# Performance work log

Measured on AMD Instinct MI355X. Metric: run time of the kernel, lower is better.

## Reference

```python
import jax, jax.numpy as jnp
import numpy as np

D_MODEL = 1024
N_HEADS = 16
D_FF = 4096
HEAD_DIM = D_MODEL // N_HEADS
LN_EPS = 1e-5


def layer_norm(x, g, b):
    m = jnp.mean(x, axis=-1, keepdims=True)
    v = jnp.mean(jnp.square(x - m), axis=-1, keepdims=True)
    return (x - m) * jax.lax.rsqrt(v + LN_EPS) * g + b


def setup_inputs() -> dict:
    key = jax.random.key(0)
    ks = jax.random.split(key, 16)
    s = 0.02
    d = {
        'x': jax.random.normal(ks[0], (4, 2048, D_MODEL), jnp.float32),
        'Wq': jax.random.normal(ks[1], (D_MODEL, D_MODEL), jnp.float32) * s,
        'bq': jnp.zeros((D_MODEL,), jnp.float32),
        'Wk': jax.random.normal(ks[2], (D_MODEL, D_MODEL), jnp.float32) * s,
        'bk': jnp.zeros((D_MODEL,), jnp.float32),
        'Wv': jax.random.normal(ks[3], (D_MODEL, D_MODEL), jnp.float32) * s,
        'bv': jnp.zeros((D_MODEL,), jnp.float32),
        'Wo': jax.random.normal(ks[4], (D_MODEL, D_MODEL), jnp.float32) * s,
        'bo': jnp.zeros((D_MODEL,), jnp.float32),
        'W1': jax.random.normal(ks[5], (D_FF, D_MODEL), jnp.float32) * s,
        'b1': jnp.zeros((D_FF,), jnp.float32),
        'W2': jax.random.normal(ks[6], (D_MODEL, D_FF), jnp.float32) * s,
        'b2': jnp.zeros((D_MODEL,), jnp.float32),
        'g1': jnp.ones((D_MODEL,), jnp.float32),
        'be1': jnp.zeros((D_MODEL,), jnp.float32),
        'g2': jnp.ones((D_MODEL,), jnp.float32),
        'be2': jnp.zeros((D_MODEL,), jnp.float32),
    }
    return d


def reference(x, Wq, bq, Wk, bk, Wv, bv, Wo, bo, W1, b1, W2, b2, g1, be1, g2, be2):
    B, S, D = x.shape
    H, hd = N_HEADS, HEAD_DIM
    # QKV projections; chunk along d_model -> heads (same as reshape last dim)
    q = (x @ Wq.T + bq).reshape(B, S, H, hd)
    k = (x @ Wk.T + bk).reshape(B, S, H, hd)
    v = (x @ Wv.T + bv).reshape(B, S, H, hd)
    # scaled dot-product attention (no mask, dropout = identity in eval)
    scores = jnp.einsum('bqhd,bkhd->bhqk', q, k) / jnp.sqrt(jnp.float32(hd))
    attn = jax.nn.softmax(scores, axis=-1)
    ctx = jnp.einsum('bhqk,bkhd->bqhd', attn, v).reshape(B, S, D)
    out1 = ctx @ Wo.T + bo
    out = layer_norm(x + out1, g1, be1)
    out2 = jax.nn.relu(out @ W1.T + b1) @ W2.T + b2
    # NOTE: faithful to source bug: second residual uses out1, not out
    return layer_norm(out1 + out2, g2, be2)
```

## Files before the change

### kernel.cpp

```cpp
#include <hip/hip_runtime.h>

typedef __bf16 bf16_t;
typedef __bf16 bf16x8 __attribute__((ext_vector_type(8)));
typedef __bf16 bf16x4 __attribute__((ext_vector_type(4)));
typedef float  f32x4  __attribute__((ext_vector_type(4)));

#define SEQ   2048
#define DMODEL 1024
#define DFF   4096
#define NHEAD 16
#define HDIM  64
#define MTOK  8192

#define MB (size_t)(1024*1024)
static const size_t XB_OFF   = 0;
static const size_t Q_OFF    = 16*MB;
static const size_t K_OFF    = 32*MB;
static const size_t VT_OFF   = 48*MB;
static const size_t FFN1_OFF = 0;
static const size_t CTX_OFF  = 64*MB;
static const size_t OUT1_OFF = 80*MB;
static const size_t LN1_OFF  = 112*MB;
static const size_t WQ_OFF   = 128*MB;
static const size_t WK_OFF   = 130*MB;
static const size_t WV_OFF   = 132*MB;
static const size_t WO_OFF   = 134*MB;
static const size_t W1_OFF   = 136*MB;
static const size_t W2_OFF   = 144*MB;

__device__ inline void gload16(const void* g, void* l) {
    __builtin_amdgcn_global_load_lds((__attribute__((address_space(1))) void*)g,
                                     (__attribute__((address_space(3))) void*)l, 16, 0, 0);
}

__global__ __launch_bounds__(256) void cast_bf16_k(const float* __restrict__ s,
                                                   bf16_t* __restrict__ d, int n8) {
    int i = blockIdx.x * 256 + threadIdx.x;
    if (i >= n8) return;
    float4 v0 = ((const float4*)s)[2*i];
    float4 v1 = ((const float4*)s)[2*i+1];
    bf16x8 o;
    o[0]=(bf16_t)v0.x; o[1]=(bf16_t)v0.y; o[2]=(bf16_t)v0.z; o[3]=(bf16_t)v0.w;
    o[4]=(bf16_t)v1.x; o[5]=(bf16_t)v1.y; o[6]=(bf16_t)v1.z; o[7]=(bf16_t)v1.w;
    *(bf16x8*)(d + (size_t)i*8) = o;
}

template<int EPI>
__global__ __launch_bounds__(256, 2) void gemm_bt(
    const bf16_t* __restrict__ A, const bf16_t* __restrict__ Bm,
    const float* __restrict__ bias, void* __restrict__ out,
    const float* __restrict__ aux, int M, int N, int K, float scale)
{
    __shared__ bf16_t As[128*64];
    __shared__ bf16_t Bs[128*64];
    const int tid = threadIdx.x;
    const int l   = tid & 63;
    const int wid = tid >> 6;
    const int wm  = wid >> 1, wn = wid & 1;
    const int c16 = l & 15,   g  = l >> 4;
    const long brow = (long)blockIdx.y * 128;
    const long bcol = (long)blockIdx.x * 128;

    f32x4 acc[4][4] = {};

    const int nkt = K >> 6;
    for (int kt = 0; kt < nkt; ++kt) {
        __syncthreads();
        const bf16_t* Ag = A  + brow * K + kt*64;
        const bf16_t* Bg = Bm + bcol * K + kt*64;
#pragma unroll
        for (int c = 0; c < 4; ++c) {
            int e   = (c*256 + tid) * 8;
            int row = e >> 6;
            int col = e & 63;
            gload16(Ag + (long)row*K + col, &As[e]);
            gload16(Bg + (long)row*K + col, &Bs[e]);
        }
        __syncthreads();
#pragma unroll
        for (int kk = 0; kk < 2; ++kk) {
            bf16x8 af[4], bfr[4];
#pragma unroll
            for (int mi = 0; mi < 4; ++mi)
                af[mi] = *(const bf16x8*)&As[(wm*64 + mi*16 + c16)*64 + kk*32 + 8*g];
#pragma unroll
            for (int ni = 0; ni < 4; ++ni)
                bfr[ni] = *(const bf16x8*)&Bs[(wn*64 + ni*16 + c16)*64 + kk*32 + 8*g];
#pragma unroll
            for (int mi = 0; mi < 4; ++mi)
#pragma unroll
                for (int ni = 0; ni < 4; ++ni)
                    acc[mi][ni] = __builtin_amdgcn_mfma_f32_16x16x32_bf16(
                        af[mi], bfr[ni], acc[mi][ni], 0, 0, 0);
        }
    }

#pragma unroll
    for (int ni = 0; ni < 4; ++ni) {
        const long c = bcol + wn*64 + ni*16 + c16;
        const float bv = bias[c];
#pragma unroll
        for (int mi = 0; mi < 4; ++mi) {
#pragma unroll
            for (int i = 0; i < 4; ++i) {
                const long r = brow + wm*64 + mi*16 + g*4 + i;
                float v = (acc[mi][ni][i] + bv) * scale;
                if constexpr (EPI == 0) {
                    long off = (((r >> 11)*NHEAD + (c >> 6))*SEQ + (r & (SEQ-1)))*HDIM + (c & 63);
                    ((bf16_t*)out)[off] = (bf16_t)v;
                } else if constexpr (EPI == 1) {
                    long off = (((r >> 11)*NHEAD + (c >> 6))*HDIM + (c & 63))*SEQ + (r & (SEQ-1));
                    ((bf16_t*)out)[off] = (bf16_t)v;
                } else if constexpr (EPI == 2) {
                    ((float*)out)[r*N + c] = v;
                } else if constexpr (EPI == 3) {
                    ((bf16_t*)out)[r*N + c] = (bf16_t)fmaxf(v, 0.f);
                } else {
                    ((float*)out)[r*N + c] = v + aux[r*N + c];
                }
            }
        }
    }
}

__device__ __forceinline__ void kload(bf16x8 (&dst)[4][2], const bf16_t* kb0,
                                      int ktt, int c16, int g) {
    const bf16_t* kbase = kb0 + (size_t)ktt*64*HDIM;
#pragma unroll
    for (int jk = 0; jk < 4; ++jk)
#pragma unroll
        for (int ks = 0; ks < 2; ++ks)
            dst[jk][ks] = *(const bf16x8*)(kbase + (size_t)(16*jk + c16)*HDIM + ks*32 + 8*g);
}

__device__ __forceinline__ void vload(bf16x8 (&vr)[4][2], const bf16_t* vt0,
                                      int ktt, int c16, int g) {
#pragma unroll
    for (int nf = 0; nf < 4; ++nf)
#pragma unroll
        for (int ks = 0; ks < 2; ++ks)
            vr[nf][ks] = *(const bf16x8*)(vt0 + (size_t)(16*nf + c16)*SEQ + ktt*64 + ks*32 + 8*g);
}

__device__ __forceinline__ void attn_step(
    const bf16x8 (&kr)[4][2], const bf16x8 (&vr)[4][2], const bf16x8 (&aq)[2][2],
    f32x4 (&acc)[2][4], float (&m)[2], float (&ls)[2],
    char* myP, int c16, int g)
{
    f32x4 s[2][4];
    const f32x4 z = {0.f, 0.f, 0.f, 0.f};
    __builtin_amdgcn_s_setprio(1);
#pragma unroll
    for (int qf = 0; qf < 2; ++qf)
#pragma unroll
        for (int jk = 0; jk < 4; ++jk) {
            s[qf][jk] = __builtin_amdgcn_mfma_f32_16x16x32_bf16(kr[jk][0], aq[qf][0], z, 0, 0, 0);
            s[qf][jk] = __builtin_amdgcn_mfma_f32_16x16x32_bf16(kr[jk][1], aq[qf][1], s[qf][jk], 0, 0, 0);
        }
    __builtin_amdgcn_s_setprio(0);
#pragma unroll
    for (int qf = 0; qf < 2; ++qf) {
        float a0 = fmaxf(fmaxf(s[qf][0][0], s[qf][0][1]), fmaxf(s[qf][0][2], s[qf][0][3]));
        float a1 = fmaxf(fmaxf(s[qf][1][0], s[qf][1][1]), fmaxf(s[qf][1][2], s[qf][1][3]));
        float a2 = fmaxf(fmaxf(s[qf][2][0], s[qf][2][1]), fmaxf(s[qf][2][2], s[qf][2][3]));
        float a3 = fmaxf(fmaxf(s[qf][3][0], s[qf][3][1]), fmaxf(s[qf][3][2], s[qf][3][3]));
        float pm = fmaxf(fmaxf(a0, a1), fmaxf(a2, a3));
        pm = fmaxf(pm, __shfl_xor(pm, 16, 64));
        pm = fmaxf(pm, __shfl_xor(pm, 32, 64));
        if (__any(pm > m[qf] + 8.0f)) {
            float mn   = fmaxf(m[qf], pm);
            float corr = __expf(m[qf] - mn);
            ls[qf] *= corr;
            m[qf]   = mn;
            float c0 = __shfl(corr, 4*g + 0, 64);
            float c1 = __shfl(corr, 4*g + 1, 64);
            float c2 = __shfl(corr, 4*g + 2, 64);
            float c3 = __shfl(corr, 4*g + 3, 64);
#pragma unroll
            for (int nf = 0; nf < 4; ++nf) {
                acc[qf][nf][0] *= c0; acc[qf][nf][1] *= c1;
                acc[qf][nf][2] *= c2; acc[qf][nf][3] *= c3;
            }
        }
        float rsum = 0.f;
#pragma unroll
        for (int jk = 0; jk < 4; ++jk)
#pragma unroll
            for (int i = 0; i < 4; ++i) {
                s[qf][jk][i] = __expf(s[qf][jk][i] - m[qf]);
                rsum += s[qf][jk][i];
            }
        rsum += __shfl_xor(rsum, 16, 64);
        rsum += __shfl_xor(rsum, 32, 64);
        ls[qf] += rsum;
    }
#pragma unroll
    for (int qf = 0; qf < 2; ++qf)
#pragma unroll
        for (int jk = 0; jk < 4; ++jk) {
            bf16x4 pk;
            pk[0]=(bf16_t)s[qf][jk][0]; pk[1]=(bf16_t)s[qf][jk][1];
            pk[2]=(bf16_t)s[qf][jk][2]; pk[3]=(bf16_t)s[qf][jk][3];
            *(bf16x4*)(myP + (qf*16 + c16)*128 + ((32*jk + 8*g) ^ ((c16 & 7) << 4))) = pk;
        }
    asm volatile("s_waitcnt lgkmcnt(0)" ::: "memory");
    __builtin_amdgcn_sched_barrier(0);
    __builtin_amdgcn_s_setprio(1);
#pragma unroll
    for (int qf = 0; qf < 2; ++qf)
#pragma unroll
        for (int ks = 0; ks < 2; ++ks) {
            bf16x8 pa = *(const bf16x8*)(myP + (qf*16 + c16)*128 + ((ks*64 + 16*g) ^ ((c16 & 7) << 4)));
#pragma unroll
            for (int nf = 0; nf < 4; ++nf)
                acc[qf][nf] = __builtin_amdgcn_mfma_f32_16x16x32_bf16(pa, vr[nf][ks], acc[qf][nf], 0, 0, 0);
        }
    __builtin_amdgcn_s_setprio(0);
    asm volatile("" ::: "memory");
}

__global__ __launch_bounds__(256, 2) void attn_k(
    const bf16_t* __restrict__ qb, const bf16_t* __restrict__ kb,
    const bf16_t* __restrict__ vt, bf16_t* __restrict__ ctx)
{
    const int bh = blockIdx.y;
    const int w  = threadIdx.x >> 6;
    const int l  = threadIdx.x & 63;
    const int c16 = l & 15, g = l >> 4;
    const int q0 = blockIdx.x*128 + w*32;

    __shared__ char Ps[4*8192];
    char* myP = &Ps[w*8192];

    bf16x8 aq[2][2];
#pragma unroll
    for (int qf = 0; qf < 2; ++qf) {
        const bf16_t* qrow = qb + ((size_t)bh*SEQ + q0 + qf*16 + c16)*HDIM;
        aq[qf][0] = *(const bf16x8*)(qrow + 8*g);
        aq[qf][1] = *(const bf16x8*)(qrow + 32 + 8*g);
    }

    const bf16_t* kb0 = kb + (size_t)bh*SEQ*HDIM;
    const bf16_t* vt0 = vt + (size_t)bh*HDIM*SEQ;

    f32x4 acc[2][4] = {};
    float m[2]  = {-1e30f, -1e30f};
    float ls[2] = {0.f, 0.f};

    bf16x8 kA[4][2], kB[4][2], vr[4][2];
    kload(kA, kb0, 0, c16, g);
    for (int kt = 0; kt < SEQ/64; kt += 2) {
        kload(kB, kb0, kt + 1, c16, g);
        vload(vr, vt0, kt, c16, g);
        attn_step(kA, vr, aq, acc, m, ls, myP + (kt & 1)*4096, c16, g);
        kload(kA, kb0, (kt + 2 < SEQ/64) ? kt + 2 : 0, c16, g);
        vload(vr, vt0, kt + 1, c16, g);
        attn_step(kB, vr, aq, acc, m, ls, myP + ((kt + 1) & 1)*4096, c16, g);
    }

    const int b = bh >> 4, h = bh & 15;
#pragma unroll
    for (int qf = 0; qf < 2; ++qf) {
        float i0 = 1.0f / __shfl(ls[qf], 4*g + 0, 64);
        float i1 = 1.0f / __shfl(ls[qf], 4*g + 1, 64);
        float i2 = 1.0f / __shfl(ls[qf], 4*g + 2, 64);
        float i3 = 1.0f / __shfl(ls[qf], 4*g + 3, 64);
#pragma unroll
        for (int nf = 0; nf < 4; ++nf) {
            long col = (size_t)h*HDIM + nf*16 + c16;
            long rb  = (size_t)b*SEQ + q0 + qf*16 + 4*g;
            ctx[(rb + 0)*DMODEL + col] = (bf16_t)(acc[qf][nf][0] * i0);
            ctx[(rb + 1)*DMODEL + col] = (bf16_t)(acc[qf][nf][1] * i1);
            ctx[(rb + 2)*DMODEL + col] = (bf16_t)(acc[qf][nf][2] * i2);
            ctx[(rb + 3)*DMODEL + col] = (bf16_t)(acc[qf][nf][3] * i3);
        }
    }
}

__global__ __launch_bounds__(256) void ln_k(
    const float* __restrict__ a, const float* __restrict__ b,
    const float* __restrict__ g, const float* __restrict__ be,
    float* __restrict__ of, bf16_t* __restrict__ ob)
{
    const long row = blockIdx.x;
    const int tid = threadIdx.x;
    float4 v = ((const float4*)(a + row*DMODEL))[tid];
    if (b) {
        float4 u = ((const float4*)(b + row*DMODEL))[tid];
        v.x += u.x; v.y += u.y; v.z += u.z; v.w += u.w;
    }
    float s = v.x + v.y + v.z + v.w;
    float q = v.x*v.x + v.y*v.y + v.z*v.z + v.w*v.w;
#pragma unroll
    for (int msk = 1; msk < 64; msk <<= 1) {
        s += __shfl_xor(s, msk, 64);
        q += __shfl_xor(q, msk, 64);
    }
    __shared__ float sb[4], qb2[4];
    int w = tid >> 6, lid = tid & 63;
    if (lid == 0) { sb[w] = s; qb2[w] = q; }
    __syncthreads();
    s = sb[0] + sb[1] + sb[2] + sb[3];
    q = qb2[0] + qb2[1] + qb2[2] + qb2[3];
    float mean = s * (1.f/1024.f);
    float var  = q * (1.f/1024.f) - mean*mean;
    float rs   = rsqrtf(var + 1e-5f);
    float4 gv = ((const float4*)g)[tid];
    float4 bv = ((const float4*)be)[tid];
    float o0 = (v.x-mean)*rs*gv.x + bv.x;
    float o1 = (v.y-mean)*rs*gv.y + bv.y;
    float o2 = (v.z-mean)*rs*gv.z + bv.z;
    float o3 = (v.w-mean)*rs*gv.w + bv.w;
    if (ob) {
        bf16x4 o; o[0]=(bf16_t)o0; o[1]=(bf16_t)o1; o[2]=(bf16_t)o2; o[3]=(bf16_t)o3;
        *(bf16x4*)(ob + row*DMODEL + tid*4) = o;
    } else {
        float4 o = make_float4(o0, o1, o2, o3);
        ((float4*)(of + row*DMODEL))[tid] = o;
    }
}

extern "C" void kernel_launch(void* const* d_in, const int* in_sizes, int n_in,
                              void* d_out, int out_size, void* d_ws, size_t ws_size,
                              hipStream_t stream)
{
    const float* x   = (const float*)d_in[0];
    const float* Wq  = (const float*)d_in[1];
    const float* bq  = (const float*)d_in[2];
    const float* Wk  = (const float*)d_in[3];
    const float* bk  = (const float*)d_in[4];
    const float* Wv  = (const float*)d_in[5];
    const float* bvv = (const float*)d_in[6];
    const float* Wo  = (const float*)d_in[7];
    const float* bo  = (const float*)d_in[8];
    const float* W1  = (const float*)d_in[9];
    const float* b1  = (const float*)d_in[10];
    const float* W2  = (const float*)d_in[11];
    const float* b2  = (const float*)d_in[12];
    const float* g1  = (const float*)d_in[13];
    const float* be1 = (const float*)d_in[14];
    const float* g2  = (const float*)d_in[15];
    const float* be2 = (const float*)d_in[16];

    char* ws = (char*)d_ws;
    bf16_t* xb   = (bf16_t*)(ws + XB_OFF);
    bf16_t* qbuf = (bf16_t*)(ws + Q_OFF);
    bf16_t* kbuf = (bf16_t*)(ws + K_OFF);
    bf16_t* vtb  = (bf16_t*)(ws + VT_OFF);
    bf16_t* ffn1 = (bf16_t*)(ws + FFN1_OFF);
    bf16_t* ctxb = (bf16_t*)(ws + CTX_OFF);
    float*  out1 = (float*)(ws + OUT1_OFF);
    bf16_t* ln1b = (bf16_t*)(ws + LN1_OFF);
    bf16_t* wqb  = (bf16_t*)(ws + WQ_OFF);
    bf16_t* wkb  = (bf16_t*)(ws + WK_OFF);
    bf16_t* wvb  = (bf16_t*)(ws + WV_OFF);
    bf16_t* wob  = (bf16_t*)(ws + WO_OFF);
    bf16_t* w1b  = (bf16_t*)(ws + W1_OFF);
    bf16_t* w2b  = (bf16_t*)(ws + W2_OFF);
    float*  dout = (float*)d_out;

    auto cast = [&](const float* s, bf16_t* d, long n) {
        int n8 = (int)(n / 8);
        cast_bf16_k<<<(n8 + 255)/256, 256, 0, stream>>>(s, d, n8);
    };
    cast(x,  xb,  (long)MTOK*DMODEL);
    cast(Wq, wqb, (long)DMODEL*DMODEL);
    cast(Wk, wkb, (long)DMODEL*DMODEL);
    cast(Wv, wvb, (long)DMODEL*DMODEL);
    cast(Wo, wob, (long)DMODEL*DMODEL);
    cast(W1, w1b, (long)DFF*DMODEL);
    cast(W2, w2b, (long)DMODEL*DFF);

    dim3 blk(256);
    gemm_bt<0><<<dim3(DMODEL/128, MTOK/128), blk, 0, stream>>>(xb, wqb, bq, qbuf, nullptr, MTOK, DMODEL, DMODEL, 0.125f);
    gemm_bt<0><<<dim3(DMODEL/128, MTOK/128), blk, 0, stream>>>(xb, wkb, bk, kbuf, nullptr, MTOK, DMODEL, DMODEL, 1.f);
    gemm_bt<1><<<dim3(DMODEL/128, MTOK/128), blk, 0, stream>>>(xb, wvb, bvv, vtb, nullptr, MTOK, DMODEL, DMODEL, 1.f);
    attn_k<<<dim3(SEQ/128, 4*NHEAD), blk, 0, stream>>>(qbuf, kbuf, vtb, ctxb);
    gemm_bt<2><<<dim3(DMODEL/128, MTOK/128), blk, 0, stream>>>(ctxb, wob, bo, out1, nullptr, MTOK, DMODEL, DMODEL, 1.f);
    ln_k<<<MTOK, blk, 0, stream>>>(x, out1, g1, be1, nullptr, ln1b);
    gemm_bt<3><<<dim3(DFF/128, MTOK/128), blk, 0, stream>>>(ln1b, w1b, b1, ffn1, nullptr, MTOK, DFF, DMODEL, 1.f);
    gemm_bt<4><<<dim3(DMODEL/128, MTOK/128), blk, 0, stream>>>(ffn1, w2b, b2, out1, out1, MTOK, DMODEL, DFF, 1.f);
    ln_k<<<MTOK, blk, 0, stream>>>(out1, nullptr, g2, be2, dout, nullptr);
}
```

Before: 585.8 us.

## Fuse QKV GEMMs, swizzle GEMM tiles, and software-pipeline attention loop

Concatenates Wq/Wk/Wv into one bf16 weight and runs a single QKV GEMM whose epilogue scatters to Q (scaled), K and transposed V, removing two launches and two re-reads of x. Every GEMM now remaps block ids so that consecutive blocks land on different XCDs. The attention kernel uses a 1D grid with a head-interleaved mapping and is restructured into a pipeline that overlaps the QK MFMAs of the next tile with the softmax and PV of the current one, double-buffering K registers. This raises register pressure in attention, and the concatenated bias is staged in the out1 buffer, which is overwritten later.

```diff
diff --git a/kernel.cpp b/kernel.cpp
--- a/kernel.cpp
+++ b/kernel.cpp
@@ -21,9 +21,7 @@
 static const size_t CTX_OFF  = 64*MB;
 static const size_t OUT1_OFF = 80*MB;
 static const size_t LN1_OFF  = 112*MB;
-static const size_t WQ_OFF   = 128*MB;
-static const size_t WK_OFF   = 130*MB;
-static const size_t WV_OFF   = 132*MB;
+static const size_t WQKV_OFF = 128*MB;
 static const size_t WO_OFF   = 134*MB;
 static const size_t W1_OFF   = 136*MB;
 static const size_t W2_OFF   = 144*MB;
@@ -45,10 +43,19 @@
     *(bf16x8*)(d + (size_t)i*8) = o;
 }
 
+__global__ __launch_bounds__(256) void concat_bias_k(const float* __restrict__ a,
+                                                     const float* __restrict__ b,
+                                                     const float* __restrict__ c,
+                                                     float* __restrict__ o) {
+    int i = blockIdx.x * 256 + threadIdx.x;
+    o[i] = (i < 1024) ? a[i] : ((i < 2048) ? b[i - 1024] : c[i - 2048]);
+}
+
 template<int EPI>
 __global__ __launch_bounds__(256, 2) void gemm_bt(
     const bf16_t* __restrict__ A, const bf16_t* __restrict__ Bm,
     const float* __restrict__ bias, void* __restrict__ out,
+    void* __restrict__ out_k, void* __restrict__ out_v,
     const float* __restrict__ aux, int M, int N, int K, float scale)
 {
     __shared__ bf16_t As[128*64];
@@ -58,8 +65,11 @@
     const int wid = tid >> 6;
     const int wm  = wid >> 1, wn = wid & 1;
     const int c16 = l & 15,   g  = l >> 4;
-    const long brow = (long)blockIdx.y * 128;
-    const long bcol = (long)blockIdx.x * 128;
+    int lin = blockIdx.y * gridDim.x + blockIdx.x;
+    int nwg = gridDim.x * gridDim.y;
+    int swz = (lin & 7) * (nwg >> 3) + (lin >> 3);
+    const long brow = (long)(swz / gridDim.x) * 128;
+    const long bcol = (long)(swz % gridDim.x) * 128;
 
     f32x4 acc[4][4] = {};
 
@@ -105,18 +115,23 @@
             for (int i = 0; i < 4; ++i) {
                 const long r = brow + wm*64 + mi*16 + g*4 + i;
                 float v = (acc[mi][ni][i] + bv) * scale;
-                if constexpr (EPI == 0) {
-                    long off = (((r >> 11)*NHEAD + (c >> 6))*SEQ + (r & (SEQ-1)))*HDIM + (c & 63);
-                    ((bf16_t*)out)[off] = (bf16_t)v;
-                } else if constexpr (EPI == 1) {
-                    long off = (((r >> 11)*NHEAD + (c >> 6))*HDIM + (c & 63))*SEQ + (r & (SEQ-1));
-                    ((bf16_t*)out)[off] = (bf16_t)v;
-                } else if constexpr (EPI == 2) {
+                if constexpr (EPI == 2) {
                     ((float*)out)[r*N + c] = v;
                 } else if constexpr (EPI == 3) {
                     ((bf16_t*)out)[r*N + c] = (bf16_t)fmaxf(v, 0.f);
-                } else {
+                } else if constexpr (EPI == 4) {
                     ((float*)out)[r*N + c] = v + aux[r*N + c];
+                } else if constexpr (EPI == 5) {
+                    const int mat = (int)(c >> 10);
+                    const int hc  = (int)(c & 1023);
+                    const long bb = r >> 11, sidx = r & (SEQ-1);
+                    const long hb = bb*NHEAD + (hc >> 6);
+                    if (mat == 0)
+                        ((bf16_t*)out)[(hb*SEQ + sidx)*HDIM + (hc & 63)] = (bf16_t)(v * 0.125f);
+                    else if (mat == 1)
+                        ((bf16_t*)out_k)[(hb*SEQ + sidx)*HDIM + (hc & 63)] = (bf16_t)v;
+                    else
+                        ((bf16_t*)out_v)[(hb*HDIM + (hc & 63))*SEQ + sidx] = (bf16_t)v;
                 }
             }
         }
@@ -142,12 +157,8 @@
             vr[nf][ks] = *(const bf16x8*)(vt0 + (size_t)(16*nf + c16)*SEQ + ktt*64 + ks*32 + 8*g);
 }
 
-__device__ __forceinline__ void attn_step(
-    const bf16x8 (&kr)[4][2], const bf16x8 (&vr)[4][2], const bf16x8 (&aq)[2][2],
-    f32x4 (&acc)[2][4], float (&m)[2], float (&ls)[2],
-    char* myP, int c16, int g)
-{
-    f32x4 s[2][4];
+__device__ __forceinline__ void qk_step(f32x4 (&s)[2][4], const bf16x8 (&kr)[4][2],
+                                        const bf16x8 (&aq)[2][2]) {
     const f32x4 z = {0.f, 0.f, 0.f, 0.f};
     __builtin_amdgcn_s_setprio(1);
 #pragma unroll
@@ -158,6 +169,10 @@
             s[qf][jk] = __builtin_amdgcn_mfma_f32_16x16x32_bf16(kr[jk][1], aq[qf][1], s[qf][jk], 0, 0, 0);
         }
     __builtin_amdgcn_s_setprio(0);
+}
+
+__device__ __forceinline__ void sm_step(f32x4 (&s)[2][4], f32x4 (&acc)[2][4],
+                                        float (&m)[2], float (&ls)[2], int g) {
 #pragma unroll
     for (int qf = 0; qf < 2; ++qf) {
         float a0 = fmaxf(fmaxf(s[qf][0][0], s[qf][0][1]), fmaxf(s[qf][0][2], s[qf][0][3]));
@@ -194,6 +209,9 @@
         rsum += __shfl_xor(rsum, 32, 64);
         ls[qf] += rsum;
     }
+}
+
+__device__ __forceinline__ void pwrite_step(const f32x4 (&s)[2][4], char* buf, int c16, int g) {
 #pragma unroll
     for (int qf = 0; qf < 2; ++qf)
 #pragma unroll
@@ -201,33 +219,37 @@
             bf16x4 pk;
             pk[0]=(bf16_t)s[qf][jk][0]; pk[1]=(bf16_t)s[qf][jk][1];
             pk[2]=(bf16_t)s[qf][jk][2]; pk[3]=(bf16_t)s[qf][jk][3];
-            *(bf16x4*)(myP + (qf*16 + c16)*128 + ((32*jk + 8*g) ^ ((c16 & 7) << 4))) = pk;
-        }
-    asm volatile("s_waitcnt lgkmcnt(0)" ::: "memory");
-    __builtin_amdgcn_sched_barrier(0);
+            *(bf16x4*)(buf + (qf*16 + c16)*128 + ((32*jk + 8*g) ^ ((c16 & 7) << 4))) = pk;
+        }
+}
+
+__device__ __forceinline__ void pv_step(f32x4 (&acc)[2][4], const bf16x8 (&vr)[4][2],
+                                        const char* buf, int c16, int g) {
     __builtin_amdgcn_s_setprio(1);
 #pragma unroll
     for (int qf = 0; qf < 2; ++qf)
 #pragma unroll
         for (int ks = 0; ks < 2; ++ks) {
-            bf16x8 pa = *(const bf16x8*)(myP + (qf*16 + c16)*128 + ((ks*64 + 16*g) ^ ((c16 & 7) << 4)));
+            bf16x8 pa = *(const bf16x8*)(buf + (qf*16 + c16)*128 + ((ks*64 + 16*g) ^ ((c16 & 7) << 4)));
 #pragma unroll
             for (int nf = 0; nf < 4; ++nf)
                 acc[qf][nf] = __builtin_amdgcn_mfma_f32_16x16x32_bf16(pa, vr[nf][ks], acc[qf][nf], 0, 0, 0);
         }
     __builtin_amdgcn_s_setprio(0);
-    asm volatile("" ::: "memory");
 }
 
 __global__ __launch_bounds__(256, 2) void attn_k(
     const bf16_t* __restrict__ qb, const bf16_t* __restrict__ kb,
     const bf16_t* __restrict__ vt, bf16_t* __restrict__ ctx)
 {
-    const int bh = blockIdx.y;
-    const int w  = threadIdx.x >> 6;
-    const int l  = threadIdx.x & 63;
+    const int id  = blockIdx.x;
+    const int idx = id >> 3;
+    const int bh  = (id & 7) + 8 * (idx & 7);
+    const int qt  = idx >> 3;
+    const int w   = threadIdx.x >> 6;
+    const int l   = threadIdx.x & 63;
     const int c16 = l & 15, g = l >> 4;
-    const int q0 = blockIdx.x*128 + w*32;
+    const int q0  = qt*128 + w*32;
 
     __shared__ char Ps[4*8192];
     char* myP = &Ps[w*8192];
@@ -247,16 +269,31 @@
     float m[2]  = {-1e30f, -1e30f};
     float ls[2] = {0.f, 0.f};
 
-    bf16x8 kA[4][2], kB[4][2], vr[4][2];
-    kload(kA, kb0, 0, c16, g);
-    for (int kt = 0; kt < SEQ/64; kt += 2) {
-        kload(kB, kb0, kt + 1, c16, g);
-        vload(vr, vt0, kt, c16, g);
-        attn_step(kA, vr, aq, acc, m, ls, myP + (kt & 1)*4096, c16, g);
-        kload(kA, kb0, (kt + 2 < SEQ/64) ? kt + 2 : 0, c16, g);
-        vload(vr, vt0, kt + 1, c16, g);
-        attn_step(kB, vr, aq, acc, m, ls, myP + ((kt + 1) & 1)*4096, c16, g);
-    }
+    bf16x8 kr[2][4][2], vr[4][2];
+    f32x4 s[2][4];
+
+    kload(kr[0], kb0, 0, c16, g);
+    vload(vr, vt0, 0, c16, g);
+    kload(kr[1], kb0, 1, c16, g);
+    qk_step(s, kr[0], aq);
+    sm_step(s, acc, m, ls, g);
+    pwrite_step(s, myP, c16, g);
+
+    const int NT = SEQ/64;
+    for (int t = 0; t < NT - 1; ++t) {
+        qk_step(s, kr[(t+1)&1], aq);
+        asm volatile("s_waitcnt lgkmcnt(0)" ::: "memory");
+        __builtin_amdgcn_sched_barrier(0);
+        if (t + 2 < NT) kload(kr[t&1], kb0, t+2, c16, g);
+        pv_step(acc, vr, myP + (t&1)*4096, c16, g);
+        vload(vr, vt0, t+1, c16, g);
+        __builtin_amdgcn_sched_barrier(0);
+        sm_step(s, acc, m, ls, g);
+        pwrite_step(s, myP + ((t+1)&1)*4096, c16, g);
+    }
+    asm volatile("s_waitcnt lgkmcnt(0)" ::: "memory");
+    __builtin_amdgcn_sched_barrier(0);
+    pv_step(acc, vr, myP + ((NT-1)&1)*4096, c16, g);
 
     const int b = bh >> 4, h = bh & 15;
 #pragma unroll
@@ -351,12 +388,11 @@
     bf16_t* ctxb = (bf16_t*)(ws + CTX_OFF);
     float*  out1 = (float*)(ws + OUT1_OFF);
     bf16_t* ln1b = (bf16_t*)(ws + LN1_OFF);
-    bf16_t* wqb  = (bf16_t*)(ws + WQ_OFF);
-    bf16_t* wkb  = (bf16_t*)(ws + WK_OFF);
-    bf16_t* wvb  = (bf16_t*)(ws + WV_OFF);
+    bf16_t* wqkv = (bf16_t*)(ws + WQKV_OFF);
     bf16_t* wob  = (bf16_t*)(ws + WO_OFF);
     bf16_t* w1b  = (bf16_t*)(ws + W1_OFF);
     bf16_t* w2b  = (bf16_t*)(ws + W2_OFF);
+    float*  biasc= (float*)(ws + OUT1_OFF);
     float*  dout = (float*)d_out;
 
     auto cast = [&](const float* s, bf16_t* d, long n) {
@@ -364,21 +400,24 @@
         cast_bf16_k<<<(n8 + 255)/256, 256, 0, stream>>>(s, d, n8);
     };
     cast(x,  xb,  (long)MTOK*DMODEL);
-    cast(Wq, wqb, (long)DMODEL*DMODEL);
-    cast(Wk, wkb, (long)DMODEL*DMODEL);
-    cast(Wv, wvb, (long)DMODEL*DMODEL);
+    cast(Wq, wqkv,                        (long)DMODEL*DMODEL);
+    cast(Wk, wqkv + (long)DMODEL*DMODEL,  (long)DMODEL*DMODEL);
+    cast(Wv, wqkv + 2L*DMODEL*DMODEL,     (long)DMODEL*DMODEL);
     cast(Wo, wob, (long)DMODEL*DMODEL);
     cast(W1, w1b, (long)DFF*DMODEL);
     cast(W2, w2b, (long)DMODEL*DFF);
+    concat_bias_k<<<12, 256, 0, stream>>>(bq, bk, bvv, biasc);
 
     dim3 blk(256);
-    gemm_bt<0><<<dim3(DMODEL/128, MTOK/128), blk, 0, stream>>>(xb, wqb, bq, qbuf, nullptr, MTOK, DMODEL, DMODEL, 0.125f);
-    gemm_bt<0><<<dim3(DMODEL/128, MTOK/128), blk, 0, stream>>>(xb, wkb, bk, kbuf, nullptr, MTOK, DMODEL, DMODEL, 1.f);
-    gemm_bt<1><<<dim3(DMODEL/128, MTOK/128), blk, 0, stream>>>(xb, wvb, bvv, vtb, nullptr, MTOK, DMODEL, DMODEL, 1.f);
-    attn_k<<<dim3(SEQ/128, 4*NHEAD), blk, 0, stream>>>(qbuf, kbuf, vtb, ctxb);
-    gemm_bt<2><<<dim3(DMODEL/128, MTOK/128), blk, 0, stream>>>(ctxb, wob, bo, out1, nullptr, MTOK, DMODEL, DMODEL, 1.f);
+    gemm_bt<5><<<dim3(3*DMODEL/128, MTOK/128), blk, 0, stream>>>(
+        xb, wqkv, biasc, qbuf, kbuf, vtb, nullptr, MTOK, 3*DMODEL, DMODEL, 1.f);
+    attn_k<<<dim3((SEQ/128) * 4*NHEAD), blk, 0, stream>>>(qbuf, kbuf, vtb, ctxb);
+    gemm_bt<2><<<dim3(DMODEL/128, MTOK/128), blk, 0, stream>>>(
+        ctxb, wob, bo, out1, nullptr, nullptr, nullptr, MTOK, DMODEL, DMODEL, 1.f);
     ln_k<<<MTOK, blk, 0, stream>>>(x, out1, g1, be1, nullptr, ln1b);
-    gemm_bt<3><<<dim3(DFF/128, MTOK/128), blk, 0, stream>>>(ln1b, w1b, b1, ffn1, nullptr, MTOK, DFF, DMODEL, 1.f);
-    gemm_bt<4><<<dim3(DMODEL/128, MTOK/128), blk, 0, stream>>>(ffn1, w2b, b2, out1, out1, MTOK, DMODEL, DFF, 1.f);
+    gemm_bt<3><<<dim3(DFF/128, MTOK/128), blk, 0, stream>>>(
+        ln1b, w1b, b1, ffn1, nullptr, nullptr, nullptr, MTOK, DFF, DMODEL, 1.f);
+    gemm_bt<4><<<dim3(DMODEL/128, MTOK/128), blk, 0, stream>>>(
+        ffn1, w2b, b2, out1, nullptr, nullptr, out1, MTOK, DMODEL, DFF, 1.f);
     ln_k<<<MTOK, blk, 0, stream>>>(out1, nullptr, g2, be2, dout, nullptr);
 }
```

Result: slower. 762.2 us (+30.1%).
